# Kernel optimization log

Measured on AMD Instinct MI355X. Metric: run time of the kernel, lower is better.

## Reference

```python
import jax, jax.numpy as jnp
import numpy as np

BS, DIM, HID, T = 4096, 64, 256, 101
GAMMA = 0.1
EPS = 1e-12  # pinverse guard for the 1x1 matrix G G^T


def setup_inputs() -> dict:
    key = jax.random.key(0)
    k0, k1, k2, k3 = jax.random.split(key, 4)
    return {
        "y0": jax.random.normal(k0, (BS, DIM), dtype=jnp.float32),
        "t": jnp.linspace(0.0, 1.0, T).astype(jnp.float32),
        "W1": jax.random.normal(k1, (DIM, HID), dtype=jnp.float32) * 0.05,
        "b1": jnp.zeros((HID,), dtype=jnp.float32),
        "W2": jax.random.normal(k2, (HID, DIM), dtype=jnp.float32) * 0.05,
        "b2": jnp.zeros((DIM,), dtype=jnp.float32),
        "wg": jax.random.normal(k3, (DIM,), dtype=jnp.float32) * 0.1,
        "bg": jnp.zeros((), dtype=jnp.float32),
    }


def reference(y0, t, W1, b1, W2, b2, wg, bg):
    # f_model: 2-layer tanh MLP (ignores t, as is common for autonomous dynamics)
    def f_model(ti, u):
        return jnp.tanh(u @ W1 + b1) @ W2 + b2  # (bs, dim)

    # g_fn: scalar constraint per sample
    def g_single(ui):
        return jnp.tanh(ui @ wg + bg)  # scalar

    def dynamic(ti, u):
        f_u = f_model(ti, u)                              # (bs, dim)
        g_u = jax.vmap(g_single)(u)                       # (bs,)
        # Torch detaches u before autograd Jacobian (create_graph keeps param path)
        G = jax.vmap(jax.grad(g_single))(jax.lax.stop_gradient(u))  # (bs, dim) == G_u row
        # F_u = G^T (G G^T)^+ ; G G^T is 1x1 -> scalar pinverse
        s = jnp.sum(G * G, axis=-1)                       # (bs,)
        pinv = jnp.where(jnp.abs(s) > EPS, 1.0 / s, 0.0)  # (bs,)
        stable = GAMMA * (g_u * pinv)[:, None] * G        # (bs, dim)
        return f_u - stable

    dt = t[1] - t[0]  # Euler solver uses constant dt

    def step(y, ti):
        y_new = y + dynamic(ti, y) * dt
        return y_new, y_new

    _, ys = jax.lax.scan(step, y0, t[:-1])
    return jnp.concatenate([y0[None], ys], axis=0)  # (T, bs, dim)
```

## Files before the change

kernel.cpp:

```cpp
#include <hip/hip_runtime.h>
#include <hip/hip_bf16.h>


#define GAMMA 0.1f
#define EPSG  1e-12f

typedef __attribute__((ext_vector_type(8))) short bf16x8;
typedef __attribute__((ext_vector_type(4))) float f32x4;

__device__ __forceinline__ float ftanh(float x) {
    float e = __expf(2.0f * x);
    return 1.0f - 2.0f * __builtin_amdgcn_rcpf(e + 1.0f);
}

__device__ __forceinline__ unsigned int f2bf(float f) {
    unsigned int u = __float_as_uint(f);
    return (u + 0x7fffu + ((u >> 16) & 1u)) >> 16;
}

__device__ __forceinline__ unsigned int pack2(float lo, float hi) {
    union { __hip_bfloat162 h; unsigned int u; } cv;
    cv.h = __float22bfloat162_rn(float2{lo, hi});
    return cv.u;
}

__device__ __forceinline__ float bflo(unsigned int p) { return __uint_as_float(p << 16); }
__device__ __forceinline__ float bfhi(unsigned int p) { return __uint_as_float(p & 0xffff0000u); }

#define BARRIER_LGKM() asm volatile("s_waitcnt lgkmcnt(0)\ns_barrier" ::: "memory")
#define FENCE_LDS() do { asm volatile("s_waitcnt lgkmcnt(0)" ::: "memory"); \
                         __builtin_amdgcn_sched_barrier(0); } while (0)

__device__ __forceinline__ int kperm(int lg, int j) {
    return lg * 4 + (j >> 1) + ((j & 1) << 4);
}

__global__ __launch_bounds__(512, 1) void snde_kernel(
    const float* __restrict__ y0, const float* __restrict__ t,
    const float* __restrict__ W1, const float* __restrict__ b1,
    const float* __restrict__ W2, const float* __restrict__ b2,
    const float* __restrict__ wg, const float* __restrict__ bgp,
    float* __restrict__ out)
{
    __shared__ unsigned int uAp[16 * 32];
    __shared__ unsigned int hp[16 * 128];
    __shared__ unsigned int fpp[8 * 16 * 32];
    __shared__ float        zs[16];

    const int tid = threadIdx.x;
    const int w   = tid >> 6;
    const int l   = tid & 63;
    const int l15 = l & 15;
    const int lg  = l >> 4;
    const int s0g = blockIdx.x * 16;

    bf16x8 B1[2][2];
    #pragma unroll
    for (int nt = 0; nt < 2; ++nt) {
        const int n = w * 32 + nt * 16 + l15;
        #pragma unroll
        for (int kt = 0; kt < 2; ++kt) {
            bf16x8 v;
            #pragma unroll
            for (int j = 0; j < 8; ++j)
                v[j] = (short)f2bf(W1[(kt * 32 + kperm(lg, j)) * 256 + n]);
            B1[nt][kt] = v;
        }
    }
    bf16x8 B2[4];
    #pragma unroll
    for (int nt = 0; nt < 4; ++nt) {
        const int n = nt * 16 + l15;
        bf16x8 v;
        #pragma unroll
        for (int j = 0; j < 8; ++j)
            v[j] = (short)f2bf(W2[(w * 32 + kperm(lg, j)) * 64 + n]);
        B2[nt] = v;
    }
    bf16x8 Bz[2];
    #pragma unroll
    for (int kt = 0; kt < 2; ++kt) {
        bf16x8 v;
        #pragma unroll
        for (int j = 0; j < 8; ++j)
            v[j] = (l15 == 0) ? (short)f2bf(wg[kt * 32 + kperm(lg, j)]) : (short)0;
        Bz[kt] = v;
    }

    float b1v[2];
    #pragma unroll
    for (int nt = 0; nt < 2; ++nt) b1v[nt] = b1[w * 32 + nt * 16 + l15];

    const int sU = tid >> 5;
    const int q  = tid & 31;
    const int hi = q >> 4;
    const int e  = q & 15;
    const int d0 = 32 * hi + e;
    const int d1 = d0 + 16;
    const float wg_0 = wg[d0], wg_1 = wg[d1];
    const float b2_0 = b2[d0], b2_1 = b2[d1];
    float wsum = wg_0 * wg_0 + wg_1 * wg_1;
    #pragma unroll
    for (int m = 1; m < 32; m <<= 1) wsum += __shfl_xor(wsum, m, 64);
    const float bg  = bgp[0];
    const float dtv = t[1] - t[0];

    #pragma unroll
    for (int j = 0; j < 4; ++j) hp[tid + 512 * j] = 0u;

    float uv0 = y0[(size_t)(s0g + sU) * 64 + d0];
    float uv1 = y0[(size_t)(s0g + sU) * 64 + d1];
    {
        uAp[(unsigned)(sU * 32 + q) ^ (((unsigned)(sU & 7)) << 2)] = pack2(uv0, uv1);
        out[(size_t)(s0g + sU) * 64 + d0] = uv0;
        out[(size_t)(s0g + sU) * 64 + d1] = uv1;
    }
    __syncthreads();

    for (int step = 0; step < 100; ++step) {
        bf16x8 A1[2];
        #pragma unroll
        for (int kt = 0; kt < 2; ++kt) {
            unsigned int boff = ((unsigned)(l15 * 128 + (kt * 16 + lg * 4) * 4))
                              ^ (((unsigned)(l15 & 7)) << 4);
            A1[kt] = *(const bf16x8*)((const char*)uAp + boff);
        }
        f32x4 acc1[2];
        #pragma unroll
        for (int nt = 0; nt < 2; ++nt) {
            acc1[nt][0] = b1v[nt]; acc1[nt][1] = b1v[nt];
            acc1[nt][2] = b1v[nt]; acc1[nt][3] = b1v[nt];
        }
        #pragma unroll
        for (int nt = 0; nt < 2; ++nt)
            #pragma unroll
            for (int kt = 0; kt < 2; ++kt)
                acc1[nt] = __builtin_amdgcn_mfma_f32_16x16x32_bf16(A1[kt], B1[nt][kt], acc1[nt], 0, 0, 0);

        if (w == 0) {
            f32x4 accz = {0.f, 0.f, 0.f, 0.f};
            #pragma unroll
            for (int kt = 0; kt < 2; ++kt)
                accz = __builtin_amdgcn_mfma_f32_16x16x32_bf16(A1[kt], Bz[kt], accz, 0, 0, 0);
            if (l15 == 0) *(f32x4*)(&zs[lg * 4]) = accz;
        }

        #pragma unroll
        for (int i = 0; i < 4; ++i) {
            const int m = lg * 4 + i;
            const unsigned int pk = pack2(ftanh(acc1[0][i]), ftanh(acc1[1][i]));
            unsigned int boff = ((unsigned)(m * 512 + (w * 16 + l15) * 4))
                              ^ (((unsigned)(m & 7)) << 4);
            *(unsigned int*)((char*)hp + boff) = pk;
        }
        FENCE_LDS();

        bf16x8 A2;
        {
            unsigned int boff = ((unsigned)(l15 * 512 + (w * 16 + lg * 4) * 4))
                              ^ (((unsigned)(l15 & 7)) << 4);
            A2 = *(const bf16x8*)((const char*)hp + boff);
        }
        f32x4 acc2[4];
        #pragma unroll
        for (int nt = 0; nt < 4; ++nt) {
            acc2[nt][0] = 0.f; acc2[nt][1] = 0.f; acc2[nt][2] = 0.f; acc2[nt][3] = 0.f;
        }
        #pragma unroll
        for (int nt = 0; nt < 4; ++nt)
            acc2[nt] = __builtin_amdgcn_mfma_f32_16x16x32_bf16(A2, B2[nt], acc2[nt], 0, 0, 0);

        #pragma unroll
        for (int i = 0; i < 4; ++i) {
            const int s = lg * 4 + i;
            const unsigned sw = ((unsigned)(s & 7)) << 2;
            const int base = w * 512 + s * 32;
            fpp[base + (((unsigned)l15) ^ sw)]        = pack2(acc2[0][i], acc2[1][i]);
            fpp[base + (((unsigned)(16 + l15)) ^ sw)] = pack2(acc2[2][i], acc2[3][i]);
        }
        BARRIER_LGKM();

        {
            const unsigned idxr = ((unsigned)q) ^ (((unsigned)(sU & 7)) << 2);
            float fs0 = 0.f, fs1 = 0.f;
            #pragma unroll
            for (int p = 0; p < 8; ++p) {
                const unsigned int pk = fpp[p * 512 + sU * 32 + idxr];
                fs0 += bflo(pk);
                fs1 += bfhi(pk);
            }
            const float zp = zs[sU];
            const float th = ftanh(zp + bg);
            const float qq = 1.0f - th * th;
            const float sg = qq * qq * wsum;
            const float pinv = (fabsf(sg) > EPSG) ? __builtin_amdgcn_rcpf(sg) : 0.0f;
            const float coef = GAMMA * th * pinv * qq;
            const float un0 = uv0 + (fs0 + b2_0 - coef * wg_0) * dtv;
            const float un1 = uv1 + (fs1 + b2_1 - coef * wg_1) * dtv;
            uv0 = un0; uv1 = un1;
            uAp[(unsigned)(sU * 32 + q) ^ (((unsigned)(sU & 7)) << 2)] = pack2(un0, un1);
            float* orow = &out[(size_t)(step + 1) * (4096 * 64) + (size_t)(s0g + sU) * 64];
            orow[d0] = un0;
            orow[d1] = un1;
        }
        BARRIER_LGKM();
    }
}

extern "C" void kernel_launch(void* const* d_in, const int* in_sizes, int n_in,
                              void* d_out, int out_size, void* d_ws, size_t ws_size,
                              hipStream_t stream) {
    const float* y0 = (const float*)d_in[0];
    const float* t  = (const float*)d_in[1];
    const float* W1 = (const float*)d_in[2];
    const float* b1 = (const float*)d_in[3];
    const float* W2 = (const float*)d_in[4];
    const float* b2 = (const float*)d_in[5];
    const float* wg = (const float*)d_in[6];
    const float* bg = (const float*)d_in[7];
    float* out = (float*)d_out;

    snde_kernel<<<dim3(256), dim3(512), 0, stream>>>(y0, t, W1, b1, W2, b2, wg, bg, out);
}
```

Measured before the change: 106.9 us.

## Restructure second GEMM so each wave owns output columns, removing cross-wave reduction

The second layer was split along K across the 8 waves, with partial sums packed to bf16 in LDS and reduced by a separate phase. Now every wave reads the full hidden tile and computes the whole K=256 product for one 16-column output tile, with waves 4-7 duplicating waves 0-3. Only waves 0-3 do the Euler update directly from the MFMA accumulators, and wave 4 precomputes the constraint coefficient. This removes the partial-sum LDS traffic and the bf16 rounding of partials, but adds a full barrier before the second GEMM, duplicated MFMA work, and more register use for the 8 A2 fragments.

```diff
diff --git a/kernel.cpp b/kernel.cpp
--- a/kernel.cpp
+++ b/kernel.cpp
@@ -24,12 +24,7 @@
     return cv.u;
 }
 
-__device__ __forceinline__ float bflo(unsigned int p) { return __uint_as_float(p << 16); }
-__device__ __forceinline__ float bfhi(unsigned int p) { return __uint_as_float(p & 0xffff0000u); }
-
 #define BARRIER_LGKM() asm volatile("s_waitcnt lgkmcnt(0)\ns_barrier" ::: "memory")
-#define FENCE_LDS() do { asm volatile("s_waitcnt lgkmcnt(0)" ::: "memory"); \
-                         __builtin_amdgcn_sched_barrier(0); } while (0)
 
 __device__ __forceinline__ int kperm(int lg, int j) {
     return lg * 4 + (j >> 1) + ((j & 1) << 4);
@@ -42,40 +37,40 @@
     const float* __restrict__ wg, const float* __restrict__ bgp,
     float* __restrict__ out)
 {
-    __shared__ unsigned int uAp[16 * 32];
-    __shared__ unsigned int hp[16 * 128];
-    __shared__ unsigned int fpp[8 * 16 * 32];
-    __shared__ float        zs[16];
+    __shared__ unsigned short uAs[16 * 64];
+    __shared__ unsigned int   hp[16 * 128];
+    __shared__ float          coefs[16];
 
     const int tid = threadIdx.x;
     const int w   = tid >> 6;
     const int l   = tid & 63;
     const int l15 = l & 15;
     const int lg  = l >> 4;
+    const int nt  = w & 3;
     const int s0g = blockIdx.x * 16;
 
     bf16x8 B1[2][2];
     #pragma unroll
-    for (int nt = 0; nt < 2; ++nt) {
-        const int n = w * 32 + nt * 16 + l15;
+    for (int ntt = 0; ntt < 2; ++ntt) {
+        const int n = w * 32 + ntt * 16 + l15;
         #pragma unroll
         for (int kt = 0; kt < 2; ++kt) {
             bf16x8 v;
             #pragma unroll
             for (int j = 0; j < 8; ++j)
-                v[j] = (short)f2bf(W1[(kt * 32 + kperm(lg, j)) * 256 + n]);
-            B1[nt][kt] = v;
-        }
-    }
-    bf16x8 B2[4];
-    #pragma unroll
-    for (int nt = 0; nt < 4; ++nt) {
+                v[j] = (short)f2bf(W1[(kt * 32 + lg * 8 + j) * 256 + n]);
+            B1[ntt][kt] = v;
+        }
+    }
+    bf16x8 B2[8];
+    #pragma unroll
+    for (int kt = 0; kt < 8; ++kt) {
         const int n = nt * 16 + l15;
         bf16x8 v;
         #pragma unroll
         for (int j = 0; j < 8; ++j)
-            v[j] = (short)f2bf(W2[(w * 32 + kperm(lg, j)) * 64 + n]);
-        B2[nt] = v;
+            v[j] = (short)f2bf(W2[(kt * 32 + kperm(lg, j)) * 64 + n]);
+        B2[kt] = v;
     }
     bf16x8 Bz[2];
     #pragma unroll
@@ -83,37 +78,32 @@
         bf16x8 v;
         #pragma unroll
         for (int j = 0; j < 8; ++j)
-            v[j] = (l15 == 0) ? (short)f2bf(wg[kt * 32 + kperm(lg, j)]) : (short)0;
+            v[j] = (l15 == 0) ? (short)f2bf(wg[kt * 32 + lg * 8 + j]) : (short)0;
         Bz[kt] = v;
     }
 
     float b1v[2];
     #pragma unroll
-    for (int nt = 0; nt < 2; ++nt) b1v[nt] = b1[w * 32 + nt * 16 + l15];
-
-    const int sU = tid >> 5;
-    const int q  = tid & 31;
-    const int hi = q >> 4;
-    const int e  = q & 15;
-    const int d0 = 32 * hi + e;
-    const int d1 = d0 + 16;
-    const float wg_0 = wg[d0], wg_1 = wg[d1];
-    const float b2_0 = b2[d0], b2_1 = b2[d1];
-    float wsum = wg_0 * wg_0 + wg_1 * wg_1;
-    #pragma unroll
-    for (int m = 1; m < 32; m <<= 1) wsum += __shfl_xor(wsum, m, 64);
+    for (int ntt = 0; ntt < 2; ++ntt) b1v[ntt] = b1[w * 32 + ntt * 16 + l15];
+    const float b2v = b2[nt * 16 + l15];
+    const float wgv = wg[nt * 16 + l15];
+    float wsum = wg[l] * wg[l];
+    #pragma unroll
+    for (int m = 1; m < 64; m <<= 1) wsum += __shfl_xor(wsum, m, 64);
     const float bg  = bgp[0];
     const float dtv = t[1] - t[0];
 
-    #pragma unroll
-    for (int j = 0; j < 4; ++j) hp[tid + 512 * j] = 0u;
-
-    float uv0 = y0[(size_t)(s0g + sU) * 64 + d0];
-    float uv1 = y0[(size_t)(s0g + sU) * 64 + d1];
-    {
-        uAp[(unsigned)(sU * 32 + q) ^ (((unsigned)(sU & 7)) << 2)] = pack2(uv0, uv1);
-        out[(size_t)(s0g + sU) * 64 + d0] = uv0;
-        out[(size_t)(s0g + sU) * 64 + d1] = uv1;
+    float uold[4];
+    if (w < 4) {
+        #pragma unroll
+        for (int i = 0; i < 4; ++i) {
+            const int s = lg * 4 + i;
+            const int c = nt * 16 + l15;
+            uold[i] = y0[(size_t)(s0g + s) * 64 + c];
+            unsigned int boff = ((unsigned)(s * 128 + c * 2)) ^ (((unsigned)(s & 7)) << 4);
+            *(unsigned short*)((char*)uAs + boff) = (unsigned short)f2bf(uold[i]);
+            out[(size_t)(s0g + s) * 64 + c] = uold[i];
+        }
     }
     __syncthreads();
 
@@ -121,28 +111,39 @@
         bf16x8 A1[2];
         #pragma unroll
         for (int kt = 0; kt < 2; ++kt) {
-            unsigned int boff = ((unsigned)(l15 * 128 + (kt * 16 + lg * 4) * 4))
+            unsigned int boff = ((unsigned)(l15 * 128 + (kt * 32 + lg * 8) * 2))
                               ^ (((unsigned)(l15 & 7)) << 4);
-            A1[kt] = *(const bf16x8*)((const char*)uAp + boff);
+            A1[kt] = *(const bf16x8*)((const char*)uAs + boff);
         }
         f32x4 acc1[2];
         #pragma unroll
-        for (int nt = 0; nt < 2; ++nt) {
-            acc1[nt][0] = b1v[nt]; acc1[nt][1] = b1v[nt];
-            acc1[nt][2] = b1v[nt]; acc1[nt][3] = b1v[nt];
-        }
-        #pragma unroll
-        for (int nt = 0; nt < 2; ++nt)
+        for (int ntt = 0; ntt < 2; ++ntt) {
+            acc1[ntt][0] = b1v[ntt]; acc1[ntt][1] = b1v[ntt];
+            acc1[ntt][2] = b1v[ntt]; acc1[ntt][3] = b1v[ntt];
+        }
+        #pragma unroll
+        for (int ntt = 0; ntt < 2; ++ntt)
             #pragma unroll
             for (int kt = 0; kt < 2; ++kt)
-                acc1[nt] = __builtin_amdgcn_mfma_f32_16x16x32_bf16(A1[kt], B1[nt][kt], acc1[nt], 0, 0, 0);
-
-        if (w == 0) {
+                acc1[ntt] = __builtin_amdgcn_mfma_f32_16x16x32_bf16(A1[kt], B1[ntt][kt], acc1[ntt], 0, 0, 0);
+
+        if (w == 4) {
             f32x4 accz = {0.f, 0.f, 0.f, 0.f};
             #pragma unroll
             for (int kt = 0; kt < 2; ++kt)
                 accz = __builtin_amdgcn_mfma_f32_16x16x32_bf16(A1[kt], Bz[kt], accz, 0, 0, 0);
-            if (l15 == 0) *(f32x4*)(&zs[lg * 4]) = accz;
+            if (l15 == 0) {
+                f32x4 cf;
+                #pragma unroll
+                for (int i = 0; i < 4; ++i) {
+                    const float th = ftanh(accz[i] + bg);
+                    const float qq = 1.0f - th * th;
+                    const float sg = qq * qq * wsum;
+                    const float pinv = (fabsf(sg) > EPSG) ? __builtin_amdgcn_rcpf(sg) : 0.0f;
+                    cf[i] = GAMMA * th * pinv * qq;
+                }
+                *(f32x4*)(&coefs[lg * 4]) = cf;
+            }
         }
 
         #pragma unroll
@@ -153,55 +154,41 @@
                               ^ (((unsigned)(m & 7)) << 4);
             *(unsigned int*)((char*)hp + boff) = pk;
         }
-        FENCE_LDS();
-
-        bf16x8 A2;
-        {
-            unsigned int boff = ((unsigned)(l15 * 512 + (w * 16 + lg * 4) * 4))
+        BARRIER_LGKM();
+
+        bf16x8 A2[8];
+        #pragma unroll
+        for (int kt = 0; kt < 8; ++kt) {
+            unsigned int boff = ((unsigned)(l15 * 512 + (kt * 16 + lg * 4) * 4))
                               ^ (((unsigned)(l15 & 7)) << 4);
-            A2 = *(const bf16x8*)((const char*)hp + boff);
-        }
-        f32x4 acc2[4];
-        #pragma unroll
-        for (int nt = 0; nt < 4; ++nt) {
-            acc2[nt][0] = 0.f; acc2[nt][1] = 0.f; acc2[nt][2] = 0.f; acc2[nt][3] = 0.f;
-        }
-        #pragma unroll
-        for (int nt = 0; nt < 4; ++nt)
-            acc2[nt] = __builtin_amdgcn_mfma_f32_16x16x32_bf16(A2, B2[nt], acc2[nt], 0, 0, 0);
-
-        #pragma unroll
-        for (int i = 0; i < 4; ++i) {
-            const int s = lg * 4 + i;
-            const unsigned sw = ((unsigned)(s & 7)) << 2;
-            const int base = w * 512 + s * 32;
-            fpp[base + (((unsigned)l15) ^ sw)]        = pack2(acc2[0][i], acc2[1][i]);
-            fpp[base + (((unsigned)(16 + l15)) ^ sw)] = pack2(acc2[2][i], acc2[3][i]);
-        }
-        BARRIER_LGKM();
-
-        {
-            const unsigned idxr = ((unsigned)q) ^ (((unsigned)(sU & 7)) << 2);
-            float fs0 = 0.f, fs1 = 0.f;
-            #pragma unroll
-            for (int p = 0; p < 8; ++p) {
-                const unsigned int pk = fpp[p * 512 + sU * 32 + idxr];
-                fs0 += bflo(pk);
-                fs1 += bfhi(pk);
+            A2[kt] = *(const bf16x8*)((const char*)hp + boff);
+        }
+        f32x4 accA, accB;
+        accA[0] = b2v; accA[1] = b2v; accA[2] = b2v; accA[3] = b2v;
+        accB[0] = 0.f; accB[1] = 0.f; accB[2] = 0.f; accB[3] = 0.f;
+        #pragma unroll
+        for (int kt = 0; kt < 4; ++kt)
+            accA = __builtin_amdgcn_mfma_f32_16x16x32_bf16(A2[kt], B2[kt], accA, 0, 0, 0);
+        #pragma unroll
+        for (int kt = 4; kt < 8; ++kt)
+            accB = __builtin_amdgcn_mfma_f32_16x16x32_bf16(A2[kt], B2[kt], accB, 0, 0, 0);
+        asm volatile("" :: "v"(accA[0]), "v"(accA[1]), "v"(accA[2]), "v"(accA[3]),
+                           "v"(accB[0]), "v"(accB[1]), "v"(accB[2]), "v"(accB[3]));
+
+        if (w < 4) {
+            const f32x4 cf = *(const f32x4*)(&coefs[lg * 4]);
+            const int c = nt * 16 + l15;
+            float* orow = &out[(size_t)(step + 1) * (4096 * 64) + (size_t)(s0g + lg * 4) * 64 + c];
+            #pragma unroll
+            for (int i = 0; i < 4; ++i) {
+                const float f  = accA[i] + accB[i];
+                const float un = uold[i] + (f - cf[i] * wgv) * dtv;
+                uold[i] = un;
+                const int s = lg * 4 + i;
+                unsigned int boff = ((unsigned)(s * 128 + c * 2)) ^ (((unsigned)(s & 7)) << 4);
+                *(unsigned short*)((char*)uAs + boff) = (unsigned short)f2bf(un);
+                orow[i * 64] = un;
             }
-            const float zp = zs[sU];
-            const float th = ftanh(zp + bg);
-            const float qq = 1.0f - th * th;
-            const float sg = qq * qq * wsum;
-            const float pinv = (fabsf(sg) > EPSG) ? __builtin_amdgcn_rcpf(sg) : 0.0f;
-            const float coef = GAMMA * th * pinv * qq;
-            const float un0 = uv0 + (fs0 + b2_0 - coef * wg_0) * dtv;
-            const float un1 = uv1 + (fs1 + b2_1 - coef * wg_1) * dtv;
-            uv0 = un0; uv1 = un1;
-            uAp[(unsigned)(sU * 32 + q) ^ (((unsigned)(sU & 7)) << 2)] = pack2(un0, un1);
-            float* orow = &out[(size_t)(step + 1) * (4096 * 64) + (size_t)(s0g + sU) * 64];
-            orow[d0] = un0;
-            orow[d1] = un1;
         }
         BARRIER_LGKM();
     }
```

Result: faster. 103.8 us (-2.8%).
